# Optimization experiments

Measured on AMD Instinct MI355X. Metric: run time of the kernel, lower is better.

The kernel has to match this reference:

```python
import jax, jax.numpy as jnp
import numpy as np

HIDDEN = 2560
NUM_HEADS = 8
NUM_KV_HEADS = 1
HEAD_DIM = 512  # is_full=True -> HEAD_DIM_FULL
MAX_HD = 512
SCALE = 1.0 / float(HEAD_DIM) ** 0.5
SEQ = 32768
SLIDE = 512
CUR_POS = 4000
RING_POS = 100


def setup_inputs() -> dict:
    key = jax.random.key(0)
    ks = jax.random.split(key, 7)
    x = jax.random.normal(ks[0], (1, HIDDEN, 1, 1), jnp.float32)
    kv_full = jax.random.normal(ks[1], (2, NUM_KV_HEADS, SEQ, MAX_HD), jnp.float32) * 0.02
    kv_sliding = jax.random.normal(ks[2], (2, NUM_KV_HEADS, SLIDE, MAX_HD), jnp.float32) * 0.02
    wq = jax.random.normal(ks[3], (NUM_HEADS * HEAD_DIM, HIDDEN), jnp.float32) * 0.02
    wk = jax.random.normal(ks[4], (NUM_KV_HEADS * HEAD_DIM, HIDDEN), jnp.float32) * 0.02
    wv = jax.random.normal(ks[5], (NUM_KV_HEADS * HEAD_DIM, HIDDEN), jnp.float32) * 0.02
    wo = jax.random.normal(ks[6], (HIDDEN, NUM_HEADS * HEAD_DIM), jnp.float32) * 0.02
    return {"x": x, "kv_sliding": kv_sliding, "kv_full": kv_full,
            "wq": wq, "wk": wk, "wv": wv, "wo": wo,
            "current_pos": CUR_POS, "ring_pos": RING_POS}


def reference(x, kv_sliding, kv_full, wq, wk, wv, wo, current_pos, ring_pos):
    # 1x1 convs on a [1,C,1,1] input are plain matvecs
    xv = x.reshape(HIDDEN)
    q = (wq @ xv).reshape(NUM_HEADS, HEAD_DIM)            # [H, D]
    k = (wk @ xv).reshape(NUM_KV_HEADS, HEAD_DIM)         # [1, D]
    v = (wv @ xv).reshape(NUM_KV_HEADS, HEAD_DIM)         # [1, D]
    # is_full=True, slot_idx=0: slice-update write into kv_full at current_pos
    kv_full = jax.lax.dynamic_update_slice(
        kv_full, k[None, :, None, :].astype(kv_full.dtype), (0, 0, current_pos, 0))
    kv_full = jax.lax.dynamic_update_slice(
        kv_full, v[None, :, None, :].astype(kv_full.dtype), (1, 0, current_pos, 0))
    k_cache = kv_full[0, 0, :, :HEAD_DIM]                 # [S, D]
    v_cache = kv_full[1, 0, :, :HEAD_DIM]                 # [S, D]
    # GQA with 1 kv head: repeat == broadcast across the H query heads
    scores = jnp.einsum('hd,sd->hs', q.astype(jnp.float32),
                        k_cache.astype(jnp.float32)) * SCALE   # [H, S]
    probs = jax.nn.softmax(scores, axis=-1)
    attn = jnp.einsum('hs,sd->hd', probs,
                      v_cache.astype(jnp.float32)).astype(x.dtype)  # [H, D]
    out = (wo @ attn.reshape(NUM_HEADS * HEAD_DIM)).reshape(1, HIDDEN, 1, 1)
    return out
```

## Files before the change

kernel.cpp:

```cpp
#include <hip/hip_runtime.h>
#include <stdint.h>

#define HIDDEN 2560
#define NHEADS 8
#define HD 512
#define QDIM (NHEADS * HD)
#define SEQ 32768
#define CHUNK 64
#define NCHUNK (SEQ / CHUNK)
#define PART_ST (8 + NHEADS * HD)
#define SCALE 0.044194173824159216f

#define WS_QKV 0
#define WS_K   4096
#define WS_V   4608
#define WS_ATT 8192
#define WS_PART 16384

__global__ __launch_bounds__(256) void qkv_gemv(
    const float* __restrict__ x,
    const float* __restrict__ wq,
    const float* __restrict__ wk,
    const float* __restrict__ wv,
    float* __restrict__ qkv) {
  const int row = blockIdx.x * 4 + (threadIdx.x >> 6);
  const int lane = threadIdx.x & 63;
  const float* w;
  if (row < QDIM) w = wq + (size_t)row * HIDDEN;
  else if (row < QDIM + HD) w = wk + (size_t)(row - QDIM) * HIDDEN;
  else w = wv + (size_t)(row - QDIM - HD) * HIDDEN;
  float acc = 0.f;
#pragma unroll
  for (int i = 0; i < 5; i++) {
    const int j = i * 512 + lane * 8;
    float4 a0 = *(const float4*)(w + j);
    float4 a1 = *(const float4*)(w + j + 4);
    float4 b0 = *(const float4*)(x + j);
    float4 b1 = *(const float4*)(x + j + 4);
    acc += a0.x * b0.x + a0.y * b0.y + a0.z * b0.z + a0.w * b0.w +
           a1.x * b1.x + a1.y * b1.y + a1.z * b1.z + a1.w * b1.w;
  }
#pragma unroll
  for (int off = 32; off > 0; off >>= 1) acc += __shfl_xor(acc, off);
  if (lane == 0) qkv[row] = acc;
}

__global__ __launch_bounds__(256) void attn_partial(
    const float* __restrict__ kvfull,
    const float* __restrict__ ws,
    const int* __restrict__ cur_pos,
    float* __restrict__ part) {
  __shared__ float sc[CHUNK][NHEADS];
  __shared__ float4 vtmp[NHEADS][128];
  const int tid = threadIdx.x;
  const int lane = tid & 63;
  const int wid = tid >> 6;
  const int cur = cur_pos[0];
  const int s0 = blockIdx.x * CHUNK;
  const float* K = kvfull;
  const float* V = kvfull + (size_t)SEQ * HD;

  float qf[NHEADS][8];
#pragma unroll
  for (int h = 0; h < NHEADS; h++) {
    float4 a = *(const float4*)(ws + WS_QKV + h * HD + lane * 8);
    float4 b = *(const float4*)(ws + WS_QKV + h * HD + lane * 8 + 4);
    qf[h][0] = a.x; qf[h][1] = a.y; qf[h][2] = a.z; qf[h][3] = a.w;
    qf[h][4] = b.x; qf[h][5] = b.y; qf[h][6] = b.z; qf[h][7] = b.w;
  }

  for (int ii = 0; ii < CHUNK / 4; ii++) {
    const int scix = wid * (CHUNK / 4) + ii;
    const int s = s0 + scix;
    const float* krow = (s == cur) ? (ws + WS_K) : (K + (size_t)s * HD);
    float4 a = *(const float4*)(krow + lane * 8);
    float4 b = *(const float4*)(krow + lane * 8 + 4);
    float kb[8] = {a.x, a.y, a.z, a.w, b.x, b.y, b.z, b.w};
    float p[NHEADS];
#pragma unroll
    for (int h = 0; h < NHEADS; h++) {
      float t = 0.f;
#pragma unroll
      for (int e = 0; e < 8; e++) t += kb[e] * qf[h][e];
      p[h] = t;
    }
#pragma unroll
    for (int off = 32; off > 0; off >>= 1) {
#pragma unroll
      for (int h = 0; h < NHEADS; h++) p[h] += __shfl_xor(p[h], off);
    }
    if (lane == 0) {
#pragma unroll
      for (int h = 0; h < NHEADS; h++) sc[scix][h] = __expf(p[h] * SCALE);
    }
  }
  __syncthreads();

  float* pb = part + (size_t)blockIdx.x * PART_ST;
  if (tid < NHEADS) {
    float lsum = 0.f;
    for (int s = 0; s < CHUNK; s++) lsum += sc[s][tid];
    pb[tid] = lsum;
  }

  const int g = tid >> 7;
  const int tl = tid & 127;
  const int d0 = tl * 4;
  float4 acc[NHEADS];
#pragma unroll
  for (int h = 0; h < NHEADS; h++) acc[h] = make_float4(0.f, 0.f, 0.f, 0.f);
  for (int sy = g * (CHUNK / 2); sy < (g + 1) * (CHUNK / 2); sy++) {
    const int s = s0 + sy;
    const float* vrow = (s == cur) ? (ws + WS_V) : (V + (size_t)s * HD);
    float4 v4 = *(const float4*)(vrow + d0);
#pragma unroll
    for (int h = 0; h < NHEADS; h++) {
      const float pp = sc[sy][h];
      acc[h].x += pp * v4.x; acc[h].y += pp * v4.y;
      acc[h].z += pp * v4.z; acc[h].w += pp * v4.w;
    }
  }
  if (g == 1) {
#pragma unroll
    for (int h = 0; h < NHEADS; h++) vtmp[h][tl] = acc[h];
  }
  __syncthreads();
  if (g == 0) {
#pragma unroll
    for (int h = 0; h < NHEADS; h++) {
      float4 o = vtmp[h][tl];
      o.x += acc[h].x; o.y += acc[h].y; o.z += acc[h].z; o.w += acc[h].w;
      *(float4*)(pb + 8 + h * HD + d0) = o;
    }
  }
}

__global__ __launch_bounds__(256) void attn_reduce(
    const float* __restrict__ part,
    float* __restrict__ attn) {
  const int h = blockIdx.x >> 4;
  const int dgrp = blockIdx.x & 15;
  const int tid = threadIdx.x;
  __shared__ float red[256];
  __shared__ float pacc[8][32];

  red[tid] = part[(size_t)tid * PART_ST + h] + part[(size_t)(tid + 256) * PART_ST + h];
  __syncthreads();
  for (int off = 128; off > 0; off >>= 1) {
    if (tid < off) red[tid] += red[tid + off];
    __syncthreads();
  }
  const float Linv = 1.f / red[0];

  const int dloc = tid & 31;
  const int bs = tid >> 5;
  const int d = dgrp * 32 + dloc;
  float acc = 0.f;
#pragma unroll 8
  for (int b = bs * (NCHUNK / 8); b < (bs + 1) * (NCHUNK / 8); b++) {
    acc += part[(size_t)b * PART_ST + 8 + h * HD + d];
  }
  pacc[bs][dloc] = acc;
  __syncthreads();
  if (tid < 32) {
    float s = ((pacc[0][tid] + pacc[1][tid]) + (pacc[2][tid] + pacc[3][tid])) +
              ((pacc[4][tid] + pacc[5][tid]) + (pacc[6][tid] + pacc[7][tid]));
    attn[h * HD + dgrp * 32 + tid] = s * Linv;
  }
}

__global__ __launch_bounds__(256) void out_gemv(
    const float* __restrict__ wo,
    const float* __restrict__ attn,
    float* __restrict__ out) {
  const int row = blockIdx.x * 4 + (threadIdx.x >> 6);
  const int lane = threadIdx.x & 63;
  const float* w = wo + (size_t)row * QDIM;
  float acc = 0.f;
#pragma unroll
  for (int i = 0; i < 8; i++) {
    const int j = i * 512 + lane * 8;
    float4 w0 = *(const float4*)(w + j);
    float4 w1 = *(const float4*)(w + j + 4);
    float4 a0 = *(const float4*)(attn + j);
    float4 a1 = *(const float4*)(attn + j + 4);
    acc += w0.x * a0.x + w0.y * a0.y + w0.z * a0.z + w0.w * a0.w +
           w1.x * a1.x + w1.y * a1.y + w1.z * a1.z + w1.w * a1.w;
  }
#pragma unroll
  for (int off = 32; off > 0; off >>= 1) acc += __shfl_xor(acc, off);
  if (lane == 0) out[row] = acc;
}

extern "C" void kernel_launch(void* const* d_in, const int* in_sizes, int n_in,
                              void* d_out, int out_size, void* d_ws, size_t ws_size,
                              hipStream_t stream) {
  (void)in_sizes; (void)n_in; (void)out_size; (void)ws_size;
  const float* x      = (const float*)d_in[0];
  const float* kvfull = (const float*)d_in[2];
  const float* wq     = (const float*)d_in[3];
  const float* wk     = (const float*)d_in[4];
  const float* wv     = (const float*)d_in[5];
  const float* wo     = (const float*)d_in[6];
  const int* cur_pos  = (const int*)d_in[7];
  float* out = (float*)d_out;
  float* ws = (float*)d_ws;

  qkv_gemv<<<(QDIM + 2 * HD) / 4, 256, 0, stream>>>(x, wq, wk, wv, ws + WS_QKV);
  attn_partial<<<NCHUNK, 256, 0, stream>>>(kvfull, ws, cur_pos, ws + WS_PART);
  attn_reduce<<<NHEADS * 16, 256, 0, stream>>>(ws + WS_PART, ws + WS_ATT);
  out_gemv<<<HIDDEN / 4, 256, 0, stream>>>(wo, ws + WS_ATT, out);
}
```

Before: 281.7 us.

## Fuse decode attention pipeline into one cooperative kernel with grid syncs

Replaces the four launches (QKV gemv, partial attention, reduce, output gemv) with a single cooperative kernel of 512 blocks that separates the phases with grid-wide syncs. Gemv rows are distributed over all waves in a strided loop. The reduce phase is redone so that each block handles 8 output dims with wave shuffles. The aim is to remove launch gaps and tail effects between kernels, at the cost of grid.sync overhead and a fixed grid size that must be fully co-resident.

```diff
diff --git a/kernel.cpp b/kernel.cpp
--- a/kernel.cpp
+++ b/kernel.cpp
@@ -1,14 +1,19 @@
 #include <hip/hip_runtime.h>
+#include <hip/hip_cooperative_groups.h>
 #include <stdint.h>
+
+namespace cg = cooperative_groups;
 
 #define HIDDEN 2560
 #define NHEADS 8
 #define HD 512
 #define QDIM (NHEADS * HD)
+#define QKVROWS (QDIM + 2 * HD)
 #define SEQ 32768
-#define CHUNK 64
-#define NCHUNK (SEQ / CHUNK)
-#define PART_ST (8 + NHEADS * HD)
+#define NBLK 512
+#define NWAVES (NBLK * 4)
+#define CHUNK (SEQ / NBLK)
+#define PART_ST (8 + QDIM)
 #define SCALE 0.044194173824159216f
 
 #define WS_QKV 0
@@ -17,179 +22,193 @@
 #define WS_ATT 8192
 #define WS_PART 16384
 
-__global__ __launch_bounds__(256) void qkv_gemv(
+__global__ __launch_bounds__(256) void fused_decode(
     const float* __restrict__ x,
+    const float* __restrict__ kvfull,
     const float* __restrict__ wq,
     const float* __restrict__ wk,
     const float* __restrict__ wv,
-    float* __restrict__ qkv) {
-  const int row = blockIdx.x * 4 + (threadIdx.x >> 6);
-  const int lane = threadIdx.x & 63;
-  const float* w;
-  if (row < QDIM) w = wq + (size_t)row * HIDDEN;
-  else if (row < QDIM + HD) w = wk + (size_t)(row - QDIM) * HIDDEN;
-  else w = wv + (size_t)(row - QDIM - HD) * HIDDEN;
-  float acc = 0.f;
-#pragma unroll
-  for (int i = 0; i < 5; i++) {
-    const int j = i * 512 + lane * 8;
-    float4 a0 = *(const float4*)(w + j);
-    float4 a1 = *(const float4*)(w + j + 4);
-    float4 b0 = *(const float4*)(x + j);
-    float4 b1 = *(const float4*)(x + j + 4);
-    acc += a0.x * b0.x + a0.y * b0.y + a0.z * b0.z + a0.w * b0.w +
-           a1.x * b1.x + a1.y * b1.y + a1.z * b1.z + a1.w * b1.w;
-  }
-#pragma unroll
-  for (int off = 32; off > 0; off >>= 1) acc += __shfl_xor(acc, off);
-  if (lane == 0) qkv[row] = acc;
-}
-
-__global__ __launch_bounds__(256) void attn_partial(
-    const float* __restrict__ kvfull,
-    const float* __restrict__ ws,
+    const float* __restrict__ wo,
     const int* __restrict__ cur_pos,
-    float* __restrict__ part) {
-  __shared__ float sc[CHUNK][NHEADS];
-  __shared__ float4 vtmp[NHEADS][128];
+    float* __restrict__ ws,
+    float* __restrict__ out)
+{
+  cg::grid_group grid = cg::this_grid();
   const int tid = threadIdx.x;
   const int lane = tid & 63;
   const int wid = tid >> 6;
-  const int cur = cur_pos[0];
-  const int s0 = blockIdx.x * CHUNK;
-  const float* K = kvfull;
-  const float* V = kvfull + (size_t)SEQ * HD;
-
-  float qf[NHEADS][8];
-#pragma unroll
-  for (int h = 0; h < NHEADS; h++) {
-    float4 a = *(const float4*)(ws + WS_QKV + h * HD + lane * 8);
-    float4 b = *(const float4*)(ws + WS_QKV + h * HD + lane * 8 + 4);
-    qf[h][0] = a.x; qf[h][1] = a.y; qf[h][2] = a.z; qf[h][3] = a.w;
-    qf[h][4] = b.x; qf[h][5] = b.y; qf[h][6] = b.z; qf[h][7] = b.w;
-  }
-
-  for (int ii = 0; ii < CHUNK / 4; ii++) {
-    const int scix = wid * (CHUNK / 4) + ii;
-    const int s = s0 + scix;
-    const float* krow = (s == cur) ? (ws + WS_K) : (K + (size_t)s * HD);
-    float4 a = *(const float4*)(krow + lane * 8);
-    float4 b = *(const float4*)(krow + lane * 8 + 4);
-    float kb[8] = {a.x, a.y, a.z, a.w, b.x, b.y, b.z, b.w};
-    float p[NHEADS];
+  const int bid = blockIdx.x;
+  const int gwave = bid * 4 + wid;
+
+  __shared__ float sc[CHUNK][NHEADS];
+  __shared__ float4 vtmp[NHEADS][128];
+  __shared__ float fin[4][12];
+
+  for (int row = gwave; row < QKVROWS; row += NWAVES) {
+    const float* w;
+    if (row < QDIM) w = wq + (size_t)row * HIDDEN;
+    else if (row < QDIM + HD) w = wk + (size_t)(row - QDIM) * HIDDEN;
+    else w = wv + (size_t)(row - QDIM - HD) * HIDDEN;
+    float acc = 0.f;
+#pragma unroll
+    for (int i = 0; i < 5; i++) {
+      const int j = i * 512 + lane * 8;
+      float4 a0 = *(const float4*)(w + j);
+      float4 a1 = *(const float4*)(w + j + 4);
+      float4 b0 = *(const float4*)(x + j);
+      float4 b1 = *(const float4*)(x + j + 4);
+      acc += a0.x * b0.x + a0.y * b0.y + a0.z * b0.z + a0.w * b0.w +
+             a1.x * b1.x + a1.y * b1.y + a1.z * b1.z + a1.w * b1.w;
+    }
+#pragma unroll
+    for (int off = 32; off > 0; off >>= 1) acc += __shfl_xor(acc, off);
+    if (lane == 0) ws[WS_QKV + row] = acc;
+  }
+
+  __threadfence();
+  grid.sync();
+
+  {
+    const int cur = cur_pos[0];
+    const int s0 = bid * CHUNK;
+    const float* K = kvfull;
+    const float* V = kvfull + (size_t)SEQ * HD;
+    float* pb = ws + WS_PART + (size_t)bid * PART_ST;
+
+    float qf[NHEADS][8];
 #pragma unroll
     for (int h = 0; h < NHEADS; h++) {
-      float t = 0.f;
-#pragma unroll
-      for (int e = 0; e < 8; e++) t += kb[e] * qf[h][e];
-      p[h] = t;
-    }
+      float4 a = *(const float4*)(ws + WS_QKV + h * HD + lane * 8);
+      float4 b = *(const float4*)(ws + WS_QKV + h * HD + lane * 8 + 4);
+      qf[h][0] = a.x; qf[h][1] = a.y; qf[h][2] = a.z; qf[h][3] = a.w;
+      qf[h][4] = b.x; qf[h][5] = b.y; qf[h][6] = b.z; qf[h][7] = b.w;
+    }
+
+    for (int ii = 0; ii < CHUNK / 4; ii++) {
+      const int scix = wid * (CHUNK / 4) + ii;
+      const int s = s0 + scix;
+      const float* krow = (s == cur) ? (ws + WS_K) : (K + (size_t)s * HD);
+      float4 a = *(const float4*)(krow + lane * 8);
+      float4 b = *(const float4*)(krow + lane * 8 + 4);
+      float kb[8] = {a.x, a.y, a.z, a.w, b.x, b.y, b.z, b.w};
+      float p[NHEADS];
+#pragma unroll
+      for (int h = 0; h < NHEADS; h++) {
+        float t = 0.f;
+#pragma unroll
+        for (int e = 0; e < 8; e++) t += kb[e] * qf[h][e];
+        p[h] = t;
+      }
+#pragma unroll
+      for (int off = 32; off > 0; off >>= 1) {
+#pragma unroll
+        for (int h = 0; h < NHEADS; h++) p[h] += __shfl_xor(p[h], off);
+      }
+      if (lane == 0) {
+#pragma unroll
+        for (int h = 0; h < NHEADS; h++) sc[scix][h] = __expf(p[h] * SCALE);
+      }
+    }
+    __syncthreads();
+
+    if (tid < NHEADS) {
+      float lsum = 0.f;
+      for (int s = 0; s < CHUNK; s++) lsum += sc[s][tid];
+      pb[tid] = lsum;
+    }
+
+    const int g = tid >> 7;
+    const int tl = tid & 127;
+    const int d0 = tl * 4;
+    float4 acc[NHEADS];
+#pragma unroll
+    for (int h = 0; h < NHEADS; h++) acc[h] = make_float4(0.f, 0.f, 0.f, 0.f);
+    for (int sy = g * (CHUNK / 2); sy < (g + 1) * (CHUNK / 2); sy++) {
+      const int s = s0 + sy;
+      const float* vrow = (s == cur) ? (ws + WS_V) : (V + (size_t)s * HD);
+      float4 v4 = *(const float4*)(vrow + d0);
+#pragma unroll
+      for (int h = 0; h < NHEADS; h++) {
+        const float pp = sc[sy][h];
+        acc[h].x += pp * v4.x; acc[h].y += pp * v4.y;
+        acc[h].z += pp * v4.z; acc[h].w += pp * v4.w;
+      }
+    }
+    if (g == 1) {
+#pragma unroll
+      for (int h = 0; h < NHEADS; h++) vtmp[h][tl] = acc[h];
+    }
+    __syncthreads();
+    if (g == 0) {
+#pragma unroll
+      for (int h = 0; h < NHEADS; h++) {
+        float4 o = vtmp[h][tl];
+        o.x += acc[h].x; o.y += acc[h].y; o.z += acc[h].z; o.w += acc[h].w;
+        *(float4*)(pb + 8 + h * HD + d0) = o;
+      }
+    }
+  }
+
+  __threadfence();
+  grid.sync();
+
+  {
+    const float* part = ws + WS_PART;
+    const int gd0 = bid * 8;
+    const int h = gd0 >> 9;
+    const float* p0 = part + (size_t)tid * PART_ST;
+    const float* p1 = p0 + (size_t)256 * PART_ST;
+    float den = p0[h] + p1[h];
+    float4 n0 = *(const float4*)(p0 + 8 + gd0);
+    float4 n1 = *(const float4*)(p0 + 8 + gd0 + 4);
+    float4 m0 = *(const float4*)(p1 + 8 + gd0);
+    float4 m1 = *(const float4*)(p1 + 8 + gd0 + 4);
+    n0.x += m0.x; n0.y += m0.y; n0.z += m0.z; n0.w += m0.w;
+    n1.x += m1.x; n1.y += m1.y; n1.z += m1.z; n1.w += m1.w;
 #pragma unroll
     for (int off = 32; off > 0; off >>= 1) {
-#pragma unroll
-      for (int h = 0; h < NHEADS; h++) p[h] += __shfl_xor(p[h], off);
+      den  += __shfl_xor(den, off);
+      n0.x += __shfl_xor(n0.x, off); n0.y += __shfl_xor(n0.y, off);
+      n0.z += __shfl_xor(n0.z, off); n0.w += __shfl_xor(n0.w, off);
+      n1.x += __shfl_xor(n1.x, off); n1.y += __shfl_xor(n1.y, off);
+      n1.z += __shfl_xor(n1.z, off); n1.w += __shfl_xor(n1.w, off);
     }
     if (lane == 0) {
-#pragma unroll
-      for (int h = 0; h < NHEADS; h++) sc[scix][h] = __expf(p[h] * SCALE);
-    }
-  }
-  __syncthreads();
-
-  float* pb = part + (size_t)blockIdx.x * PART_ST;
-  if (tid < NHEADS) {
-    float lsum = 0.f;
-    for (int s = 0; s < CHUNK; s++) lsum += sc[s][tid];
-    pb[tid] = lsum;
-  }
-
-  const int g = tid >> 7;
-  const int tl = tid & 127;
-  const int d0 = tl * 4;
-  float4 acc[NHEADS];
-#pragma unroll
-  for (int h = 0; h < NHEADS; h++) acc[h] = make_float4(0.f, 0.f, 0.f, 0.f);
-  for (int sy = g * (CHUNK / 2); sy < (g + 1) * (CHUNK / 2); sy++) {
-    const int s = s0 + sy;
-    const float* vrow = (s == cur) ? (ws + WS_V) : (V + (size_t)s * HD);
-    float4 v4 = *(const float4*)(vrow + d0);
-#pragma unroll
-    for (int h = 0; h < NHEADS; h++) {
-      const float pp = sc[sy][h];
-      acc[h].x += pp * v4.x; acc[h].y += pp * v4.y;
-      acc[h].z += pp * v4.z; acc[h].w += pp * v4.w;
-    }
-  }
-  if (g == 1) {
-#pragma unroll
-    for (int h = 0; h < NHEADS; h++) vtmp[h][tl] = acc[h];
-  }
-  __syncthreads();
-  if (g == 0) {
-#pragma unroll
-    for (int h = 0; h < NHEADS; h++) {
-      float4 o = vtmp[h][tl];
-      o.x += acc[h].x; o.y += acc[h].y; o.z += acc[h].z; o.w += acc[h].w;
-      *(float4*)(pb + 8 + h * HD + d0) = o;
-    }
-  }
-}
-
-__global__ __launch_bounds__(256) void attn_reduce(
-    const float* __restrict__ part,
-    float* __restrict__ attn) {
-  const int h = blockIdx.x >> 4;
-  const int dgrp = blockIdx.x & 15;
-  const int tid = threadIdx.x;
-  __shared__ float red[256];
-  __shared__ float pacc[8][32];
-
-  red[tid] = part[(size_t)tid * PART_ST + h] + part[(size_t)(tid + 256) * PART_ST + h];
-  __syncthreads();
-  for (int off = 128; off > 0; off >>= 1) {
-    if (tid < off) red[tid] += red[tid + off];
-    __syncthreads();
-  }
-  const float Linv = 1.f / red[0];
-
-  const int dloc = tid & 31;
-  const int bs = tid >> 5;
-  const int d = dgrp * 32 + dloc;
-  float acc = 0.f;
-#pragma unroll 8
-  for (int b = bs * (NCHUNK / 8); b < (bs + 1) * (NCHUNK / 8); b++) {
-    acc += part[(size_t)b * PART_ST + 8 + h * HD + d];
-  }
-  pacc[bs][dloc] = acc;
-  __syncthreads();
-  if (tid < 32) {
-    float s = ((pacc[0][tid] + pacc[1][tid]) + (pacc[2][tid] + pacc[3][tid])) +
-              ((pacc[4][tid] + pacc[5][tid]) + (pacc[6][tid] + pacc[7][tid]));
-    attn[h * HD + dgrp * 32 + tid] = s * Linv;
-  }
-}
-
-__global__ __launch_bounds__(256) void out_gemv(
-    const float* __restrict__ wo,
-    const float* __restrict__ attn,
-    float* __restrict__ out) {
-  const int row = blockIdx.x * 4 + (threadIdx.x >> 6);
-  const int lane = threadIdx.x & 63;
-  const float* w = wo + (size_t)row * QDIM;
-  float acc = 0.f;
-#pragma unroll
-  for (int i = 0; i < 8; i++) {
-    const int j = i * 512 + lane * 8;
-    float4 w0 = *(const float4*)(w + j);
-    float4 w1 = *(const float4*)(w + j + 4);
-    float4 a0 = *(const float4*)(attn + j);
-    float4 a1 = *(const float4*)(attn + j + 4);
-    acc += w0.x * a0.x + w0.y * a0.y + w0.z * a0.z + w0.w * a0.w +
-           w1.x * a1.x + w1.y * a1.y + w1.z * a1.z + w1.w * a1.w;
-  }
-#pragma unroll
-  for (int off = 32; off > 0; off >>= 1) acc += __shfl_xor(acc, off);
-  if (lane == 0) out[row] = acc;
+      fin[wid][0] = n0.x; fin[wid][1] = n0.y; fin[wid][2] = n0.z; fin[wid][3] = n0.w;
+      fin[wid][4] = n1.x; fin[wid][5] = n1.y; fin[wid][6] = n1.z; fin[wid][7] = n1.w;
+      fin[wid][8] = den;
+    }
+    __syncthreads();
+    if (tid < 9) {
+      fin[0][tid] = fin[0][tid] + fin[1][tid] + fin[2][tid] + fin[3][tid];
+    }
+    __syncthreads();
+    if (tid < 8) ws[WS_ATT + gd0 + tid] = fin[0][tid] / fin[0][8];
+  }
+
+  __threadfence();
+  grid.sync();
+
+  {
+    const float* attn = ws + WS_ATT;
+    for (int row = gwave; row < HIDDEN; row += NWAVES) {
+      const float* w = wo + (size_t)row * QDIM;
+      float acc = 0.f;
+#pragma unroll
+      for (int i = 0; i < 8; i++) {
+        const int j = i * 512 + lane * 8;
+        float4 w0 = *(const float4*)(w + j);
+        float4 w1 = *(const float4*)(w + j + 4);
+        float4 a0 = *(const float4*)(attn + j);
+        float4 a1 = *(const float4*)(attn + j + 4);
+        acc += w0.x * a0.x + w0.y * a0.y + w0.z * a0.z + w0.w * a0.w +
+               w1.x * a1.x + w1.y * a1.y + w1.z * a1.z + w1.w * a1.w;
+      }
+#pragma unroll
+      for (int off = 32; off > 0; off >>= 1) acc += __shfl_xor(acc, off);
+      if (lane == 0) out[row] = acc;
+    }
+  }
 }
 
 extern "C" void kernel_launch(void* const* d_in, const int* in_sizes, int n_in,
@@ -204,10 +223,10 @@
   const float* wo     = (const float*)d_in[6];
   const int* cur_pos  = (const int*)d_in[7];
   float* out = (float*)d_out;
-  float* ws = (float*)d_ws;
-
-  qkv_gemv<<<(QDIM + 2 * HD) / 4, 256, 0, stream>>>(x, wq, wk, wv, ws + WS_QKV);
-  attn_partial<<<NCHUNK, 256, 0, stream>>>(kvfull, ws, cur_pos, ws + WS_PART);
-  attn_reduce<<<NHEADS * 16, 256, 0, stream>>>(ws + WS_PART, ws + WS_ATT);
-  out_gemv<<<HIDDEN / 4, 256, 0, stream>>>(wo, ws + WS_ATT, out);
+  float* ws  = (float*)d_ws;
+
+  void* args[] = {(void*)&x, (void*)&kvfull, (void*)&wq, (void*)&wk, (void*)&wv,
+                  (void*)&wo, (void*)&cur_pos, (void*)&ws, (void*)&out};
+  hipLaunchCooperativeKernel((const void*)fused_decode, dim3(NBLK), dim3(256),
+                             args, 0, stream);
 }
```

After: 600.9 us. +113.3%, slower.

## Halve attention chunk size and process two K rows per iteration

Applied to the files above, without the earlier changes.

Halves the sequence chunk per block, so the attention-partial kernel launches twice as many blocks, for more parallelism across CUs. The score loop now handles two K rows per iteration, interleaving their dot products and shuffle reductions to raise instruction-level parallelism. The reduce kernel is updated to sum four partial denominators per thread to match the larger chunk count. In exchange, the partial buffer doubles in size, which adds write traffic and extra read work in the reduce step.

```diff
diff --git a/kernel.cpp b/kernel.cpp
--- a/kernel.cpp
+++ b/kernel.cpp
@@ -6,7 +6,7 @@
 #define HD 512
 #define QDIM (NHEADS * HD)
 #define SEQ 32768
-#define CHUNK 64
+#define CHUNK 32
 #define NCHUNK (SEQ / CHUNK)
 #define PART_ST (8 + NHEADS * HD)
 #define SCALE 0.044194173824159216f
@@ -69,29 +69,43 @@
     qf[h][4] = b.x; qf[h][5] = b.y; qf[h][6] = b.z; qf[h][7] = b.w;
   }
 
-  for (int ii = 0; ii < CHUNK / 4; ii++) {
-    const int scix = wid * (CHUNK / 4) + ii;
-    const int s = s0 + scix;
-    const float* krow = (s == cur) ? (ws + WS_K) : (K + (size_t)s * HD);
-    float4 a = *(const float4*)(krow + lane * 8);
-    float4 b = *(const float4*)(krow + lane * 8 + 4);
-    float kb[8] = {a.x, a.y, a.z, a.w, b.x, b.y, b.z, b.w};
-    float p[NHEADS];
+  for (int ii = 0; ii < 4; ii++) {
+    const int sx = wid * 8 + ii * 2;
+    const int sA = s0 + sx;
+    const int sB = sA + 1;
+    const float* krA = (sA == cur) ? (ws + WS_K) : (K + (size_t)sA * HD);
+    const float* krB = (sB == cur) ? (ws + WS_K) : (K + (size_t)sB * HD);
+    float4 a0 = *(const float4*)(krA + lane * 8);
+    float4 a1 = *(const float4*)(krA + lane * 8 + 4);
+    float4 b0 = *(const float4*)(krB + lane * 8);
+    float4 b1 = *(const float4*)(krB + lane * 8 + 4);
+    float kA[8] = {a0.x, a0.y, a0.z, a0.w, a1.x, a1.y, a1.z, a1.w};
+    float kB[8] = {b0.x, b0.y, b0.z, b0.w, b1.x, b1.y, b1.z, b1.w};
+    float pA[NHEADS], pB[NHEADS];
 #pragma unroll
     for (int h = 0; h < NHEADS; h++) {
-      float t = 0.f;
-#pragma unroll
-      for (int e = 0; e < 8; e++) t += kb[e] * qf[h][e];
-      p[h] = t;
+      float tA = 0.f, tB = 0.f;
+#pragma unroll
+      for (int e = 0; e < 8; e++) {
+        tA += kA[e] * qf[h][e];
+        tB += kB[e] * qf[h][e];
+      }
+      pA[h] = tA; pB[h] = tB;
     }
 #pragma unroll
     for (int off = 32; off > 0; off >>= 1) {
 #pragma unroll
-      for (int h = 0; h < NHEADS; h++) p[h] += __shfl_xor(p[h], off);
+      for (int h = 0; h < NHEADS; h++) {
+        pA[h] += __shfl_xor(pA[h], off);
+        pB[h] += __shfl_xor(pB[h], off);
+      }
     }
     if (lane == 0) {
 #pragma unroll
-      for (int h = 0; h < NHEADS; h++) sc[scix][h] = __expf(p[h] * SCALE);
+      for (int h = 0; h < NHEADS; h++) {
+        sc[sx][h]     = __expf(pA[h] * SCALE);
+        sc[sx + 1][h] = __expf(pB[h] * SCALE);
+      }
     }
   }
   __syncthreads();
@@ -144,7 +158,11 @@
   __shared__ float red[256];
   __shared__ float pacc[8][32];
 
-  red[tid] = part[(size_t)tid * PART_ST + h] + part[(size_t)(tid + 256) * PART_ST + h];
+  float dsum = 0.f;
+#pragma unroll
+  for (int k = 0; k < 4; k++)
+    dsum += part[(size_t)(tid + k * 256) * PART_ST + h];
+  red[tid] = dsum;
   __syncthreads();
   for (int off = 128; off > 0; off >>= 1) {
     if (tid < off) red[tid] += red[tid + off];
```

New measurement: 286.7 us. About the same (+1.8%).

## Replace partial-buffer reduce kernel with global atomic accumulation and fold normalization into out GEMV

Applied to the files above, without the earlier changes.

Removes the attn_reduce kernel and the large per-chunk partial buffer. Each attention block now atomically adds its unnormalized numerator and softmax denominator into a small workspace that an extra qkv_gemv block zeroes, and out_gemv divides by the per-head denominator. The K-score loop is also unrolled four rows at a time to put more loads in flight. This trades a kernel launch and about 8 MB of partial traffic for heavy float atomic contention on 4096 addresses (512 blocks each adding to every element) and a nondeterministic summation order.

```diff
diff --git a/kernel.cpp b/kernel.cpp
--- a/kernel.cpp
+++ b/kernel.cpp
@@ -5,24 +5,29 @@
 #define NHEADS 8
 #define HD 512
 #define QDIM (NHEADS * HD)
+#define QKVROWS (QDIM + 2 * HD)
 #define SEQ 32768
 #define CHUNK 64
 #define NCHUNK (SEQ / CHUNK)
-#define PART_ST (8 + NHEADS * HD)
 #define SCALE 0.044194173824159216f
 
 #define WS_QKV 0
 #define WS_K   4096
 #define WS_V   4608
-#define WS_ATT 8192
-#define WS_PART 16384
+#define WS_NUM 8192
+#define WS_DEN (WS_NUM + QDIM)
+#define ACC_FLOATS (QDIM + NHEADS)
 
 __global__ __launch_bounds__(256) void qkv_gemv(
     const float* __restrict__ x,
     const float* __restrict__ wq,
     const float* __restrict__ wk,
     const float* __restrict__ wv,
-    float* __restrict__ qkv) {
+    float* __restrict__ ws) {
+  if (blockIdx.x == QKVROWS / 4) {
+    for (int i = threadIdx.x; i < ACC_FLOATS; i += 256) ws[WS_NUM + i] = 0.f;
+    return;
+  }
   const int row = blockIdx.x * 4 + (threadIdx.x >> 6);
   const int lane = threadIdx.x & 63;
   const float* w;
@@ -42,14 +47,13 @@
   }
 #pragma unroll
   for (int off = 32; off > 0; off >>= 1) acc += __shfl_xor(acc, off);
-  if (lane == 0) qkv[row] = acc;
+  if (lane == 0) ws[WS_QKV + row] = acc;
 }
 
 __global__ __launch_bounds__(256) void attn_partial(
     const float* __restrict__ kvfull,
-    const float* __restrict__ ws,
-    const int* __restrict__ cur_pos,
-    float* __restrict__ part) {
+    float* __restrict__ ws,
+    const int* __restrict__ cur_pos) {
   __shared__ float sc[CHUNK][NHEADS];
   __shared__ float4 vtmp[NHEADS][128];
   const int tid = threadIdx.x;
@@ -69,38 +73,51 @@
     qf[h][4] = b.x; qf[h][5] = b.y; qf[h][6] = b.z; qf[h][7] = b.w;
   }
 
-  for (int ii = 0; ii < CHUNK / 4; ii++) {
-    const int scix = wid * (CHUNK / 4) + ii;
-    const int s = s0 + scix;
-    const float* krow = (s == cur) ? (ws + WS_K) : (K + (size_t)s * HD);
-    float4 a = *(const float4*)(krow + lane * 8);
-    float4 b = *(const float4*)(krow + lane * 8 + 4);
-    float kb[8] = {a.x, a.y, a.z, a.w, b.x, b.y, b.z, b.w};
-    float p[NHEADS];
-#pragma unroll
-    for (int h = 0; h < NHEADS; h++) {
-      float t = 0.f;
-#pragma unroll
-      for (int e = 0; e < 8; e++) t += kb[e] * qf[h][e];
-      p[h] = t;
+  for (int ii = 0; ii < 4; ii++) {
+    const int sx = wid * 16 + ii * 4;
+    float4 A[4], B[4];
+#pragma unroll
+    for (int u = 0; u < 4; u++) {
+      const int s = s0 + sx + u;
+      const float* kr = (s == cur) ? (ws + WS_K) : (K + (size_t)s * HD);
+      A[u] = *(const float4*)(kr + lane * 8);
+      B[u] = *(const float4*)(kr + lane * 8 + 4);
+    }
+    float p[4][NHEADS];
+#pragma unroll
+    for (int u = 0; u < 4; u++) {
+      const float kb[8] = {A[u].x, A[u].y, A[u].z, A[u].w,
+                           B[u].x, B[u].y, B[u].z, B[u].w};
+#pragma unroll
+      for (int h = 0; h < NHEADS; h++) {
+        float t = 0.f;
+#pragma unroll
+        for (int e = 0; e < 8; e++) t += kb[e] * qf[h][e];
+        p[u][h] = t;
+      }
     }
 #pragma unroll
     for (int off = 32; off > 0; off >>= 1) {
 #pragma unroll
-      for (int h = 0; h < NHEADS; h++) p[h] += __shfl_xor(p[h], off);
+      for (int u = 0; u < 4; u++) {
+#pragma unroll
+        for (int h = 0; h < NHEADS; h++) p[u][h] += __shfl_xor(p[u][h], off);
+      }
     }
     if (lane == 0) {
 #pragma unroll
-      for (int h = 0; h < NHEADS; h++) sc[scix][h] = __expf(p[h] * SCALE);
+      for (int u = 0; u < 4; u++) {
+#pragma unroll
+        for (int h = 0; h < NHEADS; h++) sc[sx + u][h] = __expf(p[u][h] * SCALE);
+      }
     }
   }
   __syncthreads();
 
-  float* pb = part + (size_t)blockIdx.x * PART_ST;
   if (tid < NHEADS) {
     float lsum = 0.f;
     for (int s = 0; s < CHUNK; s++) lsum += sc[s][tid];
-    pb[tid] = lsum;
+    atomicAdd(ws + WS_DEN + tid, lsum);
   }
 
   const int g = tid >> 7;
@@ -130,62 +147,35 @@
     for (int h = 0; h < NHEADS; h++) {
       float4 o = vtmp[h][tl];
       o.x += acc[h].x; o.y += acc[h].y; o.z += acc[h].z; o.w += acc[h].w;
-      *(float4*)(pb + 8 + h * HD + d0) = o;
-    }
-  }
-}
-
-__global__ __launch_bounds__(256) void attn_reduce(
-    const float* __restrict__ part,
-    float* __restrict__ attn) {
-  const int h = blockIdx.x >> 4;
-  const int dgrp = blockIdx.x & 15;
-  const int tid = threadIdx.x;
-  __shared__ float red[256];
-  __shared__ float pacc[8][32];
-
-  red[tid] = part[(size_t)tid * PART_ST + h] + part[(size_t)(tid + 256) * PART_ST + h];
-  __syncthreads();
-  for (int off = 128; off > 0; off >>= 1) {
-    if (tid < off) red[tid] += red[tid + off];
-    __syncthreads();
-  }
-  const float Linv = 1.f / red[0];
-
-  const int dloc = tid & 31;
-  const int bs = tid >> 5;
-  const int d = dgrp * 32 + dloc;
-  float acc = 0.f;
-#pragma unroll 8
-  for (int b = bs * (NCHUNK / 8); b < (bs + 1) * (NCHUNK / 8); b++) {
-    acc += part[(size_t)b * PART_ST + 8 + h * HD + d];
-  }
-  pacc[bs][dloc] = acc;
-  __syncthreads();
-  if (tid < 32) {
-    float s = ((pacc[0][tid] + pacc[1][tid]) + (pacc[2][tid] + pacc[3][tid])) +
-              ((pacc[4][tid] + pacc[5][tid]) + (pacc[6][tid] + pacc[7][tid]));
-    attn[h * HD + dgrp * 32 + tid] = s * Linv;
+      float* dst = ws + WS_NUM + h * HD + d0;
+      atomicAdd(dst + 0, o.x);
+      atomicAdd(dst + 1, o.y);
+      atomicAdd(dst + 2, o.z);
+      atomicAdd(dst + 3, o.w);
+    }
   }
 }
 
 __global__ __launch_bounds__(256) void out_gemv(
     const float* __restrict__ wo,
-    const float* __restrict__ attn,
+    const float* __restrict__ ws,
     float* __restrict__ out) {
   const int row = blockIdx.x * 4 + (threadIdx.x >> 6);
   const int lane = threadIdx.x & 63;
   const float* w = wo + (size_t)row * QDIM;
+  const float* num = ws + WS_NUM;
+  const float* den = ws + WS_DEN;
   float acc = 0.f;
 #pragma unroll
   for (int i = 0; i < 8; i++) {
     const int j = i * 512 + lane * 8;
     float4 w0 = *(const float4*)(w + j);
     float4 w1 = *(const float4*)(w + j + 4);
-    float4 a0 = *(const float4*)(attn + j);
-    float4 a1 = *(const float4*)(attn + j + 4);
-    acc += w0.x * a0.x + w0.y * a0.y + w0.z * a0.z + w0.w * a0.w +
-           w1.x * a1.x + w1.y * a1.y + w1.z * a1.z + w1.w * a1.w;
+    float4 a0 = *(const float4*)(num + j);
+    float4 a1 = *(const float4*)(num + j + 4);
+    float t = w0.x * a0.x + w0.y * a0.y + w0.z * a0.z + w0.w * a0.w +
+              w1.x * a1.x + w1.y * a1.y + w1.z * a1.z + w1.w * a1.w;
+    acc += t / den[i];
   }
 #pragma unroll
   for (int off = 32; off > 0; off >>= 1) acc += __shfl_xor(acc, off);
@@ -206,8 +196,7 @@
   float* out = (float*)d_out;
   float* ws = (float*)d_ws;
 
-  qkv_gemv<<<(QDIM + 2 * HD) / 4, 256, 0, stream>>>(x, wq, wk, wv, ws + WS_QKV);
-  attn_partial<<<NCHUNK, 256, 0, stream>>>(kvfull, ws, cur_pos, ws + WS_PART);
-  attn_reduce<<<NHEADS * 16, 256, 0, stream>>>(ws + WS_PART, ws + WS_ATT);
-  out_gemv<<<HIDDEN / 4, 256, 0, stream>>>(wo, ws + WS_ATT, out);
-}
+  qkv_gemv<<<QKVROWS / 4 + 1, 256, 0, stream>>>(x, wq, wk, wv, ws);
+  attn_partial<<<NCHUNK, 256, 0, stream>>>(kvfull, ws, cur_pos);
+  out_gemv<<<HIDDEN / 4, 256, 0, stream>>>(wo, ws, out);
+}
```

New measurement: 322.3 us. 14.4% more time.
